# Kernel optimization log

Measured on AMD Instinct MI355X. Metric: run time of the kernel, lower is better.

Reference implementation:

```python
import jax, jax.numpy as jnp
from jax import lax
import numpy as np

DIVISOR = 2.0

def setup_inputs() -> dict:
    key = jax.random.key(0)
    k1, k2, k3, k4 = jax.random.split(key, 4)
    B, Cin, D, H, W = 64, 8, 32, 64, 64
    Cout, KD, KH, KW = 16, 3, 3, 3
    fan_in = Cin * KD * KH * KW
    bound = 1.0 / np.sqrt(fan_in)
    x = jax.random.normal(k1, (B, Cin, D, H, W), dtype=jnp.float32)
    conv_weight = jax.random.uniform(k2, (Cout, Cin, KD, KH, KW), jnp.float32, -bound, bound)
    conv_bias = jax.random.uniform(k3, (Cout,), jnp.float32, -bound, bound)
    bias = jax.random.normal(k4, (Cout, 1, 1, 1), dtype=jnp.float32) * 0.02
    return {"x": x, "conv_weight": conv_weight, "conv_bias": conv_bias, "bias": bias}

def reference(x, conv_weight, conv_bias, bias):
    # Conv3d, stride 1, no padding, groups=1  -> [B, Cout, D-2, H-2, W-2]
    y = lax.conv_general_dilated(
        x, conv_weight, window_strides=(1, 1, 1), padding='VALID',
        dimension_numbers=('NCDHW', 'OIDHW', 'NCDHW'))
    y = y + conv_bias[None, :, None, None, None]
    # Divide by constant
    y = y / DIVISOR
    # MaxPool3d(kernel=2, stride=2), floor mode (VALID drops the trailing odd row)
    y = lax.reduce_window(y, -jnp.inf, lax.max,
                          window_dimensions=(1, 1, 2, 2, 2),
                          window_strides=(1, 1, 2, 2, 2), padding='VALID')
    # AdaptiveAvgPool3d((1,1,1)) == global mean over spatial dims
    y = jnp.mean(y, axis=(2, 3, 4), keepdims=True)  # [B, Cout, 1, 1, 1]
    # Bias add (broadcast over batch)
    y = y + bias[None]
    # Sum over channel dim (sum_dim=1, no keepdim)
    return jnp.sum(y, axis=1)  # [B, 1, 1, 1]
```

## Files before the change

### kernel.cpp

```cpp
#include <hip/hip_runtime.h>

typedef __attribute__((ext_vector_type(8))) short short8;
typedef __attribute__((ext_vector_type(4))) float f32x4;
typedef unsigned int u32;

#define ROW_B 1056
#define SLOT_B 10560
#define NSLOT 4
#define CSTRIDE 131072

__device__ __forceinline__ unsigned short f2bf(float f) {
  unsigned u = __builtin_bit_cast(unsigned, f);
  u += 0x7FFFu + ((u >> 16) & 1u);
  return (unsigned short)(u >> 16);
}
__device__ __forceinline__ u32 cvtpk(float lo, float hi) {
  u32 r;
  asm("v_cvt_pk_bf16_f32 %0, %1, %2" : "=v"(r) : "v"(lo), "v"(hi));
  return r;
}

#define LBAR()                                                                \
  {                                                                           \
    asm volatile("s_waitcnt lgkmcnt(0)" ::: "memory");                        \
    __builtin_amdgcn_s_barrier();                                             \
    __builtin_amdgcn_sched_barrier(0);                                        \
  }

#define MF(ACC, H, FR, KD, KH)                                                \
  ACC[H][wt] = __builtin_amdgcn_mfma_f32_16x16x32_bf16(FR, bfragB[KD][KH],    \
                                                       ACC[H][wt], 0, 0, 0)
#define MFI(ACC, H, FR)                                                       \
  ACC[H][wt] = __builtin_amdgcn_mfma_f32_16x16x32_bf16(FR, bfragB[0][0],      \
                                                       zf4, 0, 0, 0)

#define PROC(DP, AN, AM, AO, K0, K1, K2, DOCLOSE, SAVEP, WR, LDNEXT, DOBAR)   \
  {                                                                           \
    const int dp_ = (DP);                                                     \
    const int sb_ = (dp_ & 3) * SLOT_B + rowbase;                             \
    __builtin_amdgcn_s_setprio(1);                                            \
    _Pragma("unroll") for (int wt = 0; wt < 4; ++wt) {                        \
      const short8 f0 = *(const short8*)(smem + sb_ + 0 * ROW_B + physoff[wt]); \
      const short8 f1 = *(const short8*)(smem + sb_ + 1 * ROW_B + physoff[wt]); \
      const short8 f2 = *(const short8*)(smem + sb_ + 2 * ROW_B + physoff[wt]); \
      const short8 f3 = *(const short8*)(smem + sb_ + 3 * ROW_B + physoff[wt]); \
      if (K0) {                                                               \
        MFI(AN, 0, f0); MFI(AN, 1, f1);                                       \
        MF(AN, 0, f1, 0, 1); MF(AN, 1, f2, 0, 1);                             \
        MF(AN, 0, f2, 0, 2); MF(AN, 1, f3, 0, 2);                             \
      }                                                                       \
      if (K1) {                                                               \
        MF(AM, 0, f0, 1, 0); MF(AM, 1, f1, 1, 0);                             \
        MF(AM, 0, f1, 1, 1); MF(AM, 1, f2, 1, 1);                             \
        MF(AM, 0, f2, 1, 2); MF(AM, 1, f3, 1, 2);                             \
      }                                                                       \
      if (K2) {                                                               \
        MF(AO, 0, f0, 2, 0); MF(AO, 1, f1, 2, 0);                             \
        MF(AO, 0, f1, 2, 1); MF(AO, 1, f2, 2, 1);                             \
        MF(AO, 0, f2, 2, 2); MF(AO, 1, f3, 2, 2);                             \
      }                                                                       \
    }                                                                         \
    __builtin_amdgcn_s_setprio(0);                                            \
    if (WR) stage_write(dp_ + 2);                                             \
    if (LDNEXT) stage_load(dp_ + 3);                                          \
    if (DOCLOSE) {                                                            \
      _Pragma("unroll") for (int wt = 0; wt < 4; ++wt) {                      \
        const float e01 = fmaxf(fmaxf(AO[0][wt][0], AO[0][wt][1]),            \
                                fmaxf(AO[1][wt][0], AO[1][wt][1]));           \
        const float e23 = fmaxf(fmaxf(AO[0][wt][2], AO[0][wt][3]),            \
                                fmaxf(AO[1][wt][2], AO[1][wt][3]));           \
        if (SAVEP) {                                                          \
          p01[wt] = e01; p23[wt] = e23;                                       \
        } else if (hvalid) {                                                  \
          sum += fmaxf(p01[wt], e01);                                         \
          if (!(wt == 3 && g == 3)) sum += fmaxf(p23[wt], e23);               \
        }                                                                     \
      }                                                                       \
    }                                                                         \
    if (DOBAR) LBAR()                                                         \
  }

__launch_bounds__(256, 2)
__global__ void conv_fused(const float* __restrict__ x,
                           const float* __restrict__ cw,
                           float* __restrict__ ws) {
  __shared__ __align__(16) unsigned char smem[NSLOT * SLOT_B];
  __shared__ float wsum[4];

  const int rb  = blockIdx.x;
  const int bid = (rb & 7) * 64 + (rb >> 3);
  const int b   = bid >> 3;
  const int hq  = bid & 7;
  const int h0  = hq * 8;

  const int tid  = threadIdx.x;
  const int lane = tid & 63;
  const int wid  = tid >> 6;
  const int nm   = lane & 15;
  const int g    = lane >> 4;

  const float* xb = x + (size_t)b * (8u * 32u * 64u * 64u);

  short8 bfragB[3][3];
#pragma unroll
  for (int kd = 0; kd < 3; ++kd)
#pragma unroll
    for (int kh = 0; kh < 3; ++kh) {
      short8 f;
#pragma unroll
      for (int j = 0; j < 8; ++j) {
        float v = (g < 3) ? cw[(nm * 8 + j) * 27 + kd * 9 + kh * 3 + g] : 0.f;
        f[j] = (short)f2bf(v);
      }
      bfragB[kd][kh] = f;
    }

  const int gc = (g < 3) ? g : 2;
  int physoff[4];
#pragma unroll
  for (int wt = 0; wt < 4; ++wt) physoff[wt] = (wt * 16 + nm + gc) * 16;
  const int rowbase = (2 * wid) * ROW_B;

  bool st_act[3]; int st_toff[3]; int st_off[3];
#pragma unroll
  for (int pass = 0; pass < 3; ++pass) {
    const int t = tid + pass * 256;
    bool act = (t < 640);
    int row = (t >> 6) % 10;
    const int w = t & 63;
    int h = h0 + row;
    if (h > 63) { act = false; h = 63; }
    st_act[pass]  = act;
    st_toff[pass] = h * 64 + w;
    st_off[pass]  = row * ROW_B + w * 16;
  }

  float ld[3][8];

  auto stage_load = [&](int p) {
    const int pbase = p * 4096;
#pragma unroll
    for (int pass = 0; pass < 3; ++pass) {
      if (st_act[pass]) {
        const int o = st_toff[pass] + pbase;
#pragma unroll
        for (int c = 0; c < 8; ++c)
          ld[pass][c] = (xb + (size_t)c * CSTRIDE)[o];
      }
    }
  };
  auto stage_write = [&](int p) {
    unsigned char* d = smem + (p & 3) * SLOT_B;
#pragma unroll
    for (int pass = 0; pass < 3; ++pass) {
      if (st_act[pass]) {
        uint4 v;
        v.x = cvtpk(ld[pass][0], ld[pass][1]);
        v.y = cvtpk(ld[pass][2], ld[pass][3]);
        v.z = cvtpk(ld[pass][4], ld[pass][5]);
        v.w = cvtpk(ld[pass][6], ld[pass][7]);
        *(uint4*)(d + st_off[pass]) = v;
      }
    }
  };

  const bool hvalid = !(hq == 7 && wid == 3);
  const f32x4 zf4 = {0.f, 0.f, 0.f, 0.f};
  float sum = 0.f;
  float p01[4], p23[4];
  f32x4 accA[2][4], accB[2][4], accC[2][4];

  stage_load(0); stage_write(0);
  stage_load(1); stage_write(1);
  stage_load(2);
  LBAR()

  PROC(0, accA, accB, accC, 1, 0, 0, 0, 0, 1, 1, 0)
  PROC(1, accB, accA, accC, 1, 1, 0, 0, 0, 1, 1, 1)

  for (int p0 = 2; p0 <= 20; p0 += 6) {
    PROC(p0 + 0, accC, accB, accA, 1, 1, 1, 1, 1, 1, 1, 0)
    PROC(p0 + 1, accA, accC, accB, 1, 1, 1, 1, 0, 1, 1, 1)
    PROC(p0 + 2, accB, accA, accC, 1, 1, 1, 1, 1, 1, 1, 0)
    PROC(p0 + 3, accC, accB, accA, 1, 1, 1, 1, 0, 1, 1, 1)
    PROC(p0 + 4, accA, accC, accB, 1, 1, 1, 1, 1, 1, 1, 0)
    PROC(p0 + 5, accB, accA, accC, 1, 1, 1, 1, 0, 1, 1, 1)
  }
  PROC(26, accC, accB, accA, 1, 1, 1, 1, 1, 1, 1, 0)
  PROC(27, accA, accC, accB, 1, 1, 1, 1, 0, 1, 1, 1)
  PROC(28, accB, accA, accC, 1, 1, 1, 1, 1, 1, 1, 0)
  PROC(29, accC, accB, accA, 1, 1, 1, 1, 0, 1, 0, 1)
  PROC(30, accA, accC, accB, 0, 1, 1, 1, 1, 0, 0, 0)
  PROC(31, accB, accA, accC, 0, 0, 1, 1, 0, 0, 0, 0)

#pragma unroll
  for (int off = 32; off > 0; off >>= 1) sum += __shfl_down(sum, off);
  if (lane == 0) wsum[wid] = sum;
  __syncthreads();
  if (tid == 0) ws[bid] = wsum[0] + wsum[1] + wsum[2] + wsum[3];
}

__global__ void finalize_k(const float* __restrict__ ws,
                           const float* __restrict__ cb,
                           const float* __restrict__ bias,
                           float* __restrict__ out) {
  const int b = threadIdx.x;
  float s = 0.f;
#pragma unroll
  for (int hq = 0; hq < 8; ++hq) s += ws[b * 8 + hq];
  float cbs = 0.f, bs = 0.f;
#pragma unroll
  for (int c = 0; c < 16; ++c) { cbs += cb[c]; bs += bias[c]; }
  out[b] = 0.5f * s / 14415.f + 0.5f * cbs + bs;
}

extern "C" void kernel_launch(void* const* d_in, const int* in_sizes, int n_in,
                              void* d_out, int out_size, void* d_ws, size_t ws_size,
                              hipStream_t stream) {
  const float* x    = (const float*)d_in[0];
  const float* cw   = (const float*)d_in[1];
  const float* cb   = (const float*)d_in[2];
  const float* bias = (const float*)d_in[3];
  float* out = (float*)d_out;
  float* ws  = (float*)d_ws;

  hipLaunchKernelGGL(conv_fused, dim3(512), dim3(256), 0, stream, x, cw, ws);
  hipLaunchKernelGGL(finalize_k, dim3(1), dim3(64), 0, stream, ws, cb, bias, out);
}
```

Baseline: 78.90 us.

## Software-pipeline LDS fragment reads and deepen staging by one slot

The per-depth-plane loop now interleaves the LDS fragment loads for the next width tile with the MFMA group for the current tile. It also prefetches the first tile of the next plane into a register double buffer (pfA/pfB) before the barrier. The global-to-LDS staging distance grows from two planes ahead to three, and a barrier is now placed after every plane instead of every other one. The aim is to hide LDS read latency behind MFMAs, at the cost of more VGPRs, which may pressure the 2-blocks-per-CU occupancy target, plus extra barriers.

```diff
diff --git a/kernel.cpp b/kernel.cpp
--- a/kernel.cpp
+++ b/kernel.cpp
@@ -27,49 +27,68 @@
     __builtin_amdgcn_sched_barrier(0);                                        \
   }
 
-#define MF(ACC, H, FR, KD, KH)                                                \
-  ACC[H][wt] = __builtin_amdgcn_mfma_f32_16x16x32_bf16(FR, bfragB[KD][KH],    \
-                                                       ACC[H][wt], 0, 0, 0)
-#define MFI(ACC, H, FR)                                                       \
-  ACC[H][wt] = __builtin_amdgcn_mfma_f32_16x16x32_bf16(FR, bfragB[0][0],      \
-                                                       zf4, 0, 0, 0)
-
-#define PROC(DP, AN, AM, AO, K0, K1, K2, DOCLOSE, SAVEP, WR, LDNEXT, DOBAR)   \
+#define MFMA1(A, B, C) __builtin_amdgcn_mfma_f32_16x16x32_bf16(A, B, C, 0, 0, 0)
+
+#define RDF(SB, WT, R) (*(const short8*)(smem + (SB) + (R) * ROW_B + physoff[WT]))
+
+#define MGRP(F0, F1, F2, F3, WT, AN, AM, AO, K0, K1, K2)                      \
   {                                                                           \
-    const int dp_ = (DP);                                                     \
-    const int sb_ = (dp_ & 3) * SLOT_B + rowbase;                             \
+    if (K0) {                                                                 \
+      AN[0][WT] = MFMA1(F0, bfragB[0][0], zf4);                               \
+      AN[1][WT] = MFMA1(F1, bfragB[0][0], zf4);                               \
+      AN[0][WT] = MFMA1(F1, bfragB[0][1], AN[0][WT]);                         \
+      AN[1][WT] = MFMA1(F2, bfragB[0][1], AN[1][WT]);                         \
+      AN[0][WT] = MFMA1(F2, bfragB[0][2], AN[0][WT]);                         \
+      AN[1][WT] = MFMA1(F3, bfragB[0][2], AN[1][WT]);                         \
+    }                                                                         \
+    if (K1) {                                                                 \
+      AM[0][WT] = MFMA1(F0, bfragB[1][0], AM[0][WT]);                         \
+      AM[1][WT] = MFMA1(F1, bfragB[1][0], AM[1][WT]);                         \
+      AM[0][WT] = MFMA1(F1, bfragB[1][1], AM[0][WT]);                         \
+      AM[1][WT] = MFMA1(F2, bfragB[1][1], AM[1][WT]);                         \
+      AM[0][WT] = MFMA1(F2, bfragB[1][2], AM[0][WT]);                         \
+      AM[1][WT] = MFMA1(F3, bfragB[1][2], AM[1][WT]);                         \
+    }                                                                         \
+    if (K2) {                                                                 \
+      AO[0][WT] = MFMA1(F0, bfragB[2][0], AO[0][WT]);                         \
+      AO[1][WT] = MFMA1(F1, bfragB[2][0], AO[1][WT]);                         \
+      AO[0][WT] = MFMA1(F1, bfragB[2][1], AO[0][WT]);                         \
+      AO[1][WT] = MFMA1(F2, bfragB[2][1], AO[1][WT]);                         \
+      AO[0][WT] = MFMA1(F2, bfragB[2][2], AO[0][WT]);                         \
+      AO[1][WT] = MFMA1(F3, bfragB[2][2], AO[1][WT]);                         \
+    }                                                                         \
+  }
+
+#define PROC(DP, AN, AM, AO, PFC, PFN, K0, K1, K2, CL, SV, WR, LD, PF, BAR)   \
+  {                                                                           \
+    const int dp_  = (DP);                                                    \
+    const int sb_  = (dp_ & 3) * SLOT_B + rowbase;                            \
+    const int sbn_ = ((dp_ + 1) & 3) * SLOT_B + rowbase;                      \
+    short8 t1_0 = RDF(sb_, 1, 0), t1_1 = RDF(sb_, 1, 1),                      \
+           t1_2 = RDF(sb_, 1, 2), t1_3 = RDF(sb_, 1, 3);                      \
     __builtin_amdgcn_s_setprio(1);                                            \
-    _Pragma("unroll") for (int wt = 0; wt < 4; ++wt) {                        \
-      const short8 f0 = *(const short8*)(smem + sb_ + 0 * ROW_B + physoff[wt]); \
-      const short8 f1 = *(const short8*)(smem + sb_ + 1 * ROW_B + physoff[wt]); \
-      const short8 f2 = *(const short8*)(smem + sb_ + 2 * ROW_B + physoff[wt]); \
-      const short8 f3 = *(const short8*)(smem + sb_ + 3 * ROW_B + physoff[wt]); \
-      if (K0) {                                                               \
-        MFI(AN, 0, f0); MFI(AN, 1, f1);                                       \
-        MF(AN, 0, f1, 0, 1); MF(AN, 1, f2, 0, 1);                             \
-        MF(AN, 0, f2, 0, 2); MF(AN, 1, f3, 0, 2);                             \
-      }                                                                       \
-      if (K1) {                                                               \
-        MF(AM, 0, f0, 1, 0); MF(AM, 1, f1, 1, 0);                             \
-        MF(AM, 0, f1, 1, 1); MF(AM, 1, f2, 1, 1);                             \
-        MF(AM, 0, f2, 1, 2); MF(AM, 1, f3, 1, 2);                             \
-      }                                                                       \
-      if (K2) {                                                               \
-        MF(AO, 0, f0, 2, 0); MF(AO, 1, f1, 2, 0);                             \
-        MF(AO, 0, f1, 2, 1); MF(AO, 1, f2, 2, 1);                             \
-        MF(AO, 0, f2, 2, 2); MF(AO, 1, f3, 2, 2);                             \
-      }                                                                       \
-    }                                                                         \
+    MGRP(PFC[0], PFC[1], PFC[2], PFC[3], 0, AN, AM, AO, K0, K1, K2);          \
+    short8 t2_0 = RDF(sb_, 2, 0), t2_1 = RDF(sb_, 2, 1),                      \
+           t2_2 = RDF(sb_, 2, 2), t2_3 = RDF(sb_, 2, 3);                      \
+    MGRP(t1_0, t1_1, t1_2, t1_3, 1, AN, AM, AO, K0, K1, K2);                  \
+    short8 t3_0 = RDF(sb_, 3, 0), t3_1 = RDF(sb_, 3, 1),                      \
+           t3_2 = RDF(sb_, 3, 2), t3_3 = RDF(sb_, 3, 3);                      \
+    MGRP(t2_0, t2_1, t2_2, t2_3, 2, AN, AM, AO, K0, K1, K2);                  \
+    if (PF) {                                                                 \
+      PFN[0] = RDF(sbn_, 0, 0); PFN[1] = RDF(sbn_, 0, 1);                     \
+      PFN[2] = RDF(sbn_, 0, 2); PFN[3] = RDF(sbn_, 0, 3);                     \
+    }                                                                         \
+    MGRP(t3_0, t3_1, t3_2, t3_3, 3, AN, AM, AO, K0, K1, K2);                  \
     __builtin_amdgcn_s_setprio(0);                                            \
-    if (WR) stage_write(dp_ + 2);                                             \
-    if (LDNEXT) stage_load(dp_ + 3);                                          \
-    if (DOCLOSE) {                                                            \
+    if (WR) stage_write(dp_ + 3);                                             \
+    if (LD) stage_load(dp_ + 4);                                              \
+    if (CL) {                                                                 \
       _Pragma("unroll") for (int wt = 0; wt < 4; ++wt) {                      \
         const float e01 = fmaxf(fmaxf(AO[0][wt][0], AO[0][wt][1]),            \
                                 fmaxf(AO[1][wt][0], AO[1][wt][1]));           \
         const float e23 = fmaxf(fmaxf(AO[0][wt][2], AO[0][wt][3]),            \
                                 fmaxf(AO[1][wt][2], AO[1][wt][3]));           \
-        if (SAVEP) {                                                          \
+        if (SV) {                                                             \
           p01[wt] = e01; p23[wt] = e23;                                       \
         } else if (hvalid) {                                                  \
           sum += fmaxf(p01[wt], e01);                                         \
@@ -77,7 +96,7 @@
         }                                                                     \
       }                                                                       \
     }                                                                         \
-    if (DOBAR) LBAR()                                                         \
+    if (BAR) LBAR()                                                           \
   }
 
 __launch_bounds__(256, 2)
@@ -169,29 +188,36 @@
   float sum = 0.f;
   float p01[4], p23[4];
   f32x4 accA[2][4], accB[2][4], accC[2][4];
+  short8 pfA[4], pfB[4];
 
   stage_load(0); stage_write(0);
   stage_load(1); stage_write(1);
-  stage_load(2);
+  stage_load(2); stage_write(2);
+  stage_load(3);
   LBAR()
-
-  PROC(0, accA, accB, accC, 1, 0, 0, 0, 0, 1, 1, 0)
-  PROC(1, accB, accA, accC, 1, 1, 0, 0, 0, 1, 1, 1)
+  {
+    const int pb_ = 0 * SLOT_B + rowbase;
+    pfA[0] = RDF(pb_, 0, 0); pfA[1] = RDF(pb_, 0, 1);
+    pfA[2] = RDF(pb_, 0, 2); pfA[3] = RDF(pb_, 0, 3);
+  }
+
+  PROC(0, accA, accB, accC, pfA, pfB, 1, 0, 0, 0, 0, 1, 1, 1, 1)
+  PROC(1, accB, accA, accC, pfB, pfA, 1, 1, 0, 0, 0, 1, 1, 1, 1)
 
   for (int p0 = 2; p0 <= 20; p0 += 6) {
-    PROC(p0 + 0, accC, accB, accA, 1, 1, 1, 1, 1, 1, 1, 0)
-    PROC(p0 + 1, accA, accC, accB, 1, 1, 1, 1, 0, 1, 1, 1)
-    PROC(p0 + 2, accB, accA, accC, 1, 1, 1, 1, 1, 1, 1, 0)
-    PROC(p0 + 3, accC, accB, accA, 1, 1, 1, 1, 0, 1, 1, 1)
-    PROC(p0 + 4, accA, accC, accB, 1, 1, 1, 1, 1, 1, 1, 0)
-    PROC(p0 + 5, accB, accA, accC, 1, 1, 1, 1, 0, 1, 1, 1)
-  }
-  PROC(26, accC, accB, accA, 1, 1, 1, 1, 1, 1, 1, 0)
-  PROC(27, accA, accC, accB, 1, 1, 1, 1, 0, 1, 1, 1)
-  PROC(28, accB, accA, accC, 1, 1, 1, 1, 1, 1, 1, 0)
-  PROC(29, accC, accB, accA, 1, 1, 1, 1, 0, 1, 0, 1)
-  PROC(30, accA, accC, accB, 0, 1, 1, 1, 1, 0, 0, 0)
-  PROC(31, accB, accA, accC, 0, 0, 1, 1, 0, 0, 0, 0)
+    PROC(p0 + 0, accC, accB, accA, pfA, pfB, 1, 1, 1, 1, 1, 1, 1, 1, 1)
+    PROC(p0 + 1, accA, accC, accB, pfB, pfA, 1, 1, 1, 1, 0, 1, 1, 1, 1)
+    PROC(p0 + 2, accB, accA, accC, pfA, pfB, 1, 1, 1, 1, 1, 1, 1, 1, 1)
+    PROC(p0 + 3, accC, accB, accA, pfB, pfA, 1, 1, 1, 1, 0, 1, 1, 1, 1)
+    PROC(p0 + 4, accA, accC, accB, pfA, pfB, 1, 1, 1, 1, 1, 1, 1, 1, 1)
+    PROC(p0 + 5, accB, accA, accC, pfB, pfA, 1, 1, 1, 1, 0, 1, 1, 1, 1)
+  }
+  PROC(26, accC, accB, accA, pfA, pfB, 1, 1, 1, 1, 1, 1, 1, 1, 1)
+  PROC(27, accA, accC, accB, pfB, pfA, 1, 1, 1, 1, 0, 1, 1, 1, 1)
+  PROC(28, accB, accA, accC, pfA, pfB, 1, 1, 1, 1, 1, 1, 0, 1, 1)
+  PROC(29, accC, accB, accA, pfB, pfA, 1, 1, 1, 1, 0, 0, 0, 1, 1)
+  PROC(30, accA, accC, accB, pfA, pfB, 0, 1, 1, 1, 1, 0, 0, 1, 1)
+  PROC(31, accB, accA, accC, pfB, pfA, 0, 0, 1, 1, 0, 0, 0, 0, 0)
 
 #pragma unroll
   for (int off = 32; off > 0; off >>= 1) sum += __shfl_down(sum, off);
```

New measurement: 90.70 us. 15.0% more time.
